# Performance work log

Hardware: AMD Instinct MI355X
Metric: run time of the kernel (lower is better)

The kernel has to match this reference:

```python
import jax, jax.numpy as jnp
import numpy as np

# Material / problem parameters (from init_kwargs)
G_C = 0.0027
L_0 = 0.015
PF_TOL = 0.01
ENERGY_SCALING = 1.0
NU = 0.3
E_MOD = 210.0
LAM = E_MOD * NU / ((1.0 + NU) * (1.0 - 2.0 * NU))
MU = E_MOD / (2.0 * (1.0 + NU))
K_MOD = LAM + 2.0 * MU / 3.0  # bulk modulus for vol/dev split

N_NODES = 263169
N_ELEMS = 262144
N_IP = 4
NN = 4  # nodes per element


def setup_inputs() -> dict:
    key = jax.random.key(0)
    ks = jax.random.split(key, 9)
    u = jax.random.normal(ks[0], (N_NODES,), dtype=jnp.float32) * 0.01
    v = jax.random.normal(ks[1], (N_NODES,), dtype=jnp.float32) * 0.01
    c = jax.random.uniform(ks[2], (N_NODES,), dtype=jnp.float32)
    prev_c = jax.random.uniform(ks[3], (N_NODES,), dtype=jnp.float32)
    connectivities = jax.random.randint(ks[4], (N_ELEMS, NN), 0, N_NODES, dtype=jnp.int32)
    N = jax.random.uniform(ks[5], (N_ELEMS, N_IP, NN), dtype=jnp.float32)
    N = N / jnp.sum(N, axis=-1, keepdims=True)  # shape functions sum to 1
    dNdx = jax.random.normal(ks[6], (N_ELEMS, N_IP, 2, NN), dtype=jnp.float32)
    B = jax.random.normal(ks[7], (N_ELEMS, N_IP, 3, 2 * NN), dtype=jnp.float32)
    volumes = jax.random.uniform(ks[8], (N_ELEMS, N_IP), dtype=jnp.float32)
    return {"u": u, "v": v, "c": c, "prev_c": prev_c,
            "connectivities": connectivities, "N": N, "dNdx": dNdx,
            "B": B, "volumes": volumes}


def reference(u, v, c, prev_c, connectivities, N, dNdx, B, volumes):
    # --- phase-field gather + degradation -------------------------------
    c_el = c[connectivities]                     # [E, nn] irregular gather
    one_minus_c_el = 1.0 - c_el                  # c_elemental in source
    one_minus_c_ip = jnp.einsum('ein,en->ei', N, one_minus_c_el)  # [E, ip]
    ip_g = one_minus_c_ip ** 2                   # degradation g = (1-c)^2

    # --- fracture (AT2) energy density ----------------------------------
    c_ip = 1.0 - one_minus_c_ip
    grad_c = jnp.einsum('eidn,en->eid', dNdx, c_el)  # [E, ip, 2]
    frac_density = (G_C / (2.0 * L_0)) * (c_ip ** 2 + (L_0 ** 2) * jnp.sum(grad_c ** 2, axis=-1))
    E_fracture = jnp.sum(frac_density * volumes)

    # --- irreversibility penalty ----------------------------------------
    penalty = G_C / L_0 * (1.0 / PF_TOL ** 2 - 1.0) * ENERGY_SCALING
    E_irr = jnp.sum(0.5 * penalty * jax.nn.relu(prev_c - c) ** 2)

    # --- B-matrix strain transform --------------------------------------
    u_el = u[connectivities]                     # [E, nn]
    v_el = v[connectivities]                     # [E, nn]
    uv = jnp.stack((u_el, v_el), axis=-1).reshape(u_el.shape[0], 2 * NN)  # interleaved dofs
    strain = jnp.einsum('eikn,en->eik', B, uv)   # Voigt [E, ip, 3]
    exx, eyy, gxy = strain[..., 0], strain[..., 1], strain[..., 2]
    exy = 0.5 * gxy
    tr = exx + eyy                               # plane strain: ezz = 0

    # --- vol/dev (Amor) split energy parts ------------------------------
    dev_xx = exx - tr / 3.0
    dev_yy = eyy - tr / 3.0
    dev_zz = -tr / 3.0
    dev2 = dev_xx ** 2 + dev_yy ** 2 + dev_zz ** 2 + 2.0 * exy ** 2
    tr_pos = jnp.maximum(tr, 0.0)
    tr_neg = jnp.minimum(tr, 0.0)
    psi_plus = 0.5 * K_MOD * tr_pos ** 2 + MU * dev2
    psi_minus = 0.5 * K_MOD * tr_neg ** 2

    ip_strain_energy = (psi_plus * ip_g + psi_minus) * volumes
    E_elastic = jnp.sum(ip_strain_energy)
    return (E_elastic, E_fracture, E_irr)
```

## Files before the change

### kernel.cpp

```cpp
#include <hip/hip_runtime.h>

namespace {
constexpr int N_ELEMS  = 262144;
constexpr int N_NODES  = 263169;
constexpr int BLK      = 256;
constexpr int EPB      = 64;
constexpr int NBLOCKS  = N_ELEMS / EPB;

constexpr float GC_2L0  = 0.09f;
constexpr float L0SQ    = 0.015f * 0.015f;
constexpr float MU_     = 80.76923076923077f;
constexpr float K_MOD   = 175.0f;
constexpr float PENALTY = 1799.82f;
}

typedef float vfloat4 __attribute__((ext_vector_type(4)));

__device__ __forceinline__ float waveReduce(float x) {
#pragma unroll
    for (int off = 32; off; off >>= 1) x += __shfl_down(x, off, 64);
    return x;
}

__global__ __launch_bounds__(256) void fused_energy(
    const float* __restrict__ u, const float* __restrict__ v,
    const float* __restrict__ c, const float* __restrict__ prev_c,
    const int* __restrict__ conn,
    const float* __restrict__ Nf, const float* __restrict__ dNdx,
    const float* __restrict__ B, const float* __restrict__ vol,
    float* __restrict__ partials)
{
    __shared__ vfloat4 ldsB[24 * 65];
    __shared__ vfloat4 ldsD[2 * 257];
    __shared__ float   ldsN[12 * 66];

    const int k     = threadIdx.x;
    const int ebase = blockIdx.x * EPB;
    const long long t = (long long)blockIdx.x * BLK + k;

    const vfloat4* Bg = reinterpret_cast<const vfloat4*>(B) + (long long)ebase * 24;
#pragma unroll
    for (int r = 0; r < 6; ++r) {
        const int j = k + BLK * r;
        ldsB[(j % 24) * 65 + (j / 24)] = Bg[j];
    }

    const vfloat4* Dg = reinterpret_cast<const vfloat4*>(dNdx) + (long long)ebase * 8;
#pragma unroll
    for (int r = 0; r < 2; ++r) {
        const int j = k + BLK * r;
        ldsD[(j & 1) * 257 + (j >> 1)] = Dg[j];
    }

    const int m  = k >> 2;
    const int ip = k & 3;
    const int idx = conn[4ll * ebase + k];
    ldsN[ip * 66 + m]       = c[idx];
    ldsN[(4 + ip) * 66 + m] = u[idx];
    ldsN[(8 + ip) * 66 + m] = v[idx];

    const vfloat4 Nr  = reinterpret_cast<const vfloat4*>(Nf)[4ll * ebase + k];
    const float   vip = vol[4ll * ebase + k];

    float Eirr = 0.f;
    if (t < N_NODES) {
        float d = fmaxf(prev_c[t] - c[t], 0.f);
        Eirr = 0.5f * PENALTY * d * d;
    }

    __syncthreads();

    const float c0 = ldsN[0 * 66 + m], c1 = ldsN[1 * 66 + m];
    const float c2 = ldsN[2 * 66 + m], c3 = ldsN[3 * 66 + m];
    const float u0 = ldsN[4 * 66 + m], u1 = ldsN[5 * 66 + m];
    const float u2 = ldsN[6 * 66 + m], u3 = ldsN[7 * 66 + m];
    const float v0 = ldsN[8 * 66 + m], v1 = ldsN[9 * 66 + m];
    const float v2 = ldsN[10 * 66 + m], v3 = ldsN[11 * 66 + m];

    const vfloat4 dx = ldsD[k];
    const vfloat4 dy = ldsD[257 + k];

    const vfloat4 b0 = ldsB[(6 * ip + 0) * 65 + m];
    const vfloat4 b1 = ldsB[(6 * ip + 1) * 65 + m];
    const vfloat4 b2 = ldsB[(6 * ip + 2) * 65 + m];
    const vfloat4 b3 = ldsB[(6 * ip + 3) * 65 + m];
    const vfloat4 b4 = ldsB[(6 * ip + 4) * 65 + m];
    const vfloat4 b5 = ldsB[(6 * ip + 5) * 65 + m];

    const float o0 = 1.f - c0, o1 = 1.f - c1, o2 = 1.f - c2, o3 = 1.f - c3;
    const float omc = Nr.x * o0 + Nr.y * o1 + Nr.z * o2 + Nr.w * o3;
    const float g   = omc * omc;
    const float cip = 1.f - omc;
    const float gx  = dx.x * c0 + dx.y * c1 + dx.z * c2 + dx.w * c3;
    const float gy  = dy.x * c0 + dy.y * c1 + dy.z * c2 + dy.w * c3;
    float Efr = GC_2L0 * (cip * cip + L0SQ * (gx * gx + gy * gy)) * vip;

    const float exx = b0.x * u0 + b0.y * v0 + b0.z * u1 + b0.w * v1
                    + b1.x * u2 + b1.y * v2 + b1.z * u3 + b1.w * v3;
    const float eyy = b2.x * u0 + b2.y * v0 + b2.z * u1 + b2.w * v1
                    + b3.x * u2 + b3.y * v2 + b3.z * u3 + b3.w * v3;
    const float gxy = b4.x * u0 + b4.y * v0 + b4.z * u1 + b4.w * v1
                    + b5.x * u2 + b5.y * v2 + b5.z * u3 + b5.w * v3;
    const float exy = 0.5f * gxy;
    const float tr  = exx + eyy, tr3 = tr * (1.f / 3.f);
    const float dxx = exx - tr3, dyy = eyy - tr3, dzz = -tr3;
    const float dev2 = dxx * dxx + dyy * dyy + dzz * dzz + 2.f * exy * exy;
    const float trp = fmaxf(tr, 0.f), trn = fminf(tr, 0.f);
    float Eel = ((0.5f * K_MOD * trp * trp + MU_ * dev2) * g
                 + 0.5f * K_MOD * trn * trn) * vip;

    Eel  = waveReduce(Eel);
    Efr  = waveReduce(Efr);
    Eirr = waveReduce(Eirr);
    __shared__ float sE[4], sF[4], sI[4];
    const int lane = k & 63, wid = k >> 6;
    if (lane == 0) { sE[wid] = Eel; sF[wid] = Efr; sI[wid] = Eirr; }
    __syncthreads();
    if (k == 0) {
        float* p = partials + 3ll * blockIdx.x;
        p[0] = sE[0] + sE[1] + sE[2] + sE[3];
        p[1] = sF[0] + sF[1] + sF[2] + sF[3];
        p[2] = sI[0] + sI[1] + sI[2] + sI[3];
    }
}

__global__ __launch_bounds__(256) void final_reduce(
    const float* __restrict__ partials, float* __restrict__ out)
{
    float s0 = 0.f, s1 = 0.f, s2 = 0.f;
    for (int i = threadIdx.x; i < NBLOCKS; i += 256) {
        const float* p = partials + 3ll * i;
        s0 += p[0]; s1 += p[1]; s2 += p[2];
    }
    s0 = waveReduce(s0);
    s1 = waveReduce(s1);
    s2 = waveReduce(s2);
    __shared__ float sA[4], sB[4], sC[4];
    const int lane = threadIdx.x & 63, wid = threadIdx.x >> 6;
    if (lane == 0) { sA[wid] = s0; sB[wid] = s1; sC[wid] = s2; }
    __syncthreads();
    if (threadIdx.x == 0) {
        out[0] = sA[0] + sA[1] + sA[2] + sA[3];
        out[1] = sB[0] + sB[1] + sB[2] + sB[3];
        out[2] = sC[0] + sC[1] + sC[2] + sC[3];
    }
}

extern "C" void kernel_launch(void* const* d_in, const int* in_sizes, int n_in,
                              void* d_out, int out_size, void* d_ws, size_t ws_size,
                              hipStream_t stream) {
    const float* u      = (const float*)d_in[0];
    const float* v      = (const float*)d_in[1];
    const float* c      = (const float*)d_in[2];
    const float* prev_c = (const float*)d_in[3];
    const int*   conn   = (const int*)d_in[4];
    const float* Nf     = (const float*)d_in[5];
    const float* dNdx   = (const float*)d_in[6];
    const float* B      = (const float*)d_in[7];
    const float* vol    = (const float*)d_in[8];
    float* out      = (float*)d_out;
    float* partials = (float*)d_ws;

    fused_energy<<<NBLOCKS, BLK, 0, stream>>>(
        u, v, c, prev_c, conn, Nf, dNdx, B, vol, partials);
    final_reduce<<<1, BLK, 0, stream>>>(partials, out);
}
```

Before: 47.62 us.

## Make energy kernel persistent with register-prefetched tile pipelining and shuffle-based node sharing

Launches a fixed grid of 1024 blocks, each looping over 4 element tiles. Global loads for the next tile are prefetched into registers while the current tile is computed. Gathered node values are shared across the four integration points with wave shuffles instead of LDS, and the irreversibility term uses a grid-stride loop. It also adds a calibration kernel that streams the whole B array after the reduction, which adds extra memory traffic to the timed work.

```diff
diff --git a/kernel.cpp b/kernel.cpp
--- a/kernel.cpp
+++ b/kernel.cpp
@@ -1,11 +1,15 @@
 #include <hip/hip_runtime.h>
 
 namespace {
-constexpr int N_ELEMS  = 262144;
-constexpr int N_NODES  = 263169;
-constexpr int BLK      = 256;
-constexpr int EPB      = 64;
-constexpr int NBLOCKS  = N_ELEMS / EPB;
+constexpr int       N_ELEMS = 262144;
+constexpr long long N_NODES = 263169;
+constexpr int BLK     = 256;
+constexpr int EPB     = 64;
+constexpr int TILES   = N_ELEMS / EPB;
+constexpr int PBLOCKS = 1024;
+constexpr int TPB     = TILES / PBLOCKS;
+constexpr int CBLOCKS = 1024;
+constexpr long long B_F4 = (long long)N_ELEMS * 24;
 
 constexpr float GC_2L0  = 0.09f;
 constexpr float L0SQ    = 0.015f * 0.015f;
@@ -32,82 +36,121 @@
 {
     __shared__ vfloat4 ldsB[24 * 65];
     __shared__ vfloat4 ldsD[2 * 257];
-    __shared__ float   ldsN[12 * 66];
-
-    const int k     = threadIdx.x;
-    const int ebase = blockIdx.x * EPB;
-    const long long t = (long long)blockIdx.x * BLK + k;
-
-    const vfloat4* Bg = reinterpret_cast<const vfloat4*>(B) + (long long)ebase * 24;
+
+    const int k = threadIdx.x;
+    const int tile0 = blockIdx.x * TPB;
+    const vfloat4* Bf4 = reinterpret_cast<const vfloat4*>(B);
+    const vfloat4* Df4 = reinterpret_cast<const vfloat4*>(dNdx);
+    const vfloat4* Nf4 = reinterpret_cast<const vfloat4*>(Nf);
+
+    float Eirr = 0.f;
+    for (long long n = (long long)blockIdx.x * BLK + k; n < N_NODES;
+         n += (long long)PBLOCKS * BLK) {
+        const float d = fmaxf(prev_c[n] - c[n], 0.f);
+        Eirr += 0.5f * PENALTY * d * d;
+    }
+
+    int sCn;
+    vfloat4 sB0, sB1, sB2, sB3, sB4, sB5, sD0, sD1;
+    vfloat4 sN[2];  float sVol[2];
+    float gC[2], gU[2], gV[2];
+    float Eel = 0.f, Efr = 0.f;
+
+    const int m = k >> 2, ip = k & 3, base = k & ~3;
+
+    auto compute = [&](int s) {
+        const float c0 = __shfl(gC[s], base),     c1 = __shfl(gC[s], base + 1);
+        const float c2 = __shfl(gC[s], base + 2), c3 = __shfl(gC[s], base + 3);
+        const float u0 = __shfl(gU[s], base),     u1 = __shfl(gU[s], base + 1);
+        const float u2 = __shfl(gU[s], base + 2), u3 = __shfl(gU[s], base + 3);
+        const float v0 = __shfl(gV[s], base),     v1 = __shfl(gV[s], base + 1);
+        const float v2 = __shfl(gV[s], base + 2), v3 = __shfl(gV[s], base + 3);
+
+        const vfloat4 Nr = sN[s];
+        const float  vip = sVol[s];
+        const vfloat4 dx = ldsD[k], dy = ldsD[257 + k];
+        const vfloat4 b0 = ldsB[(6 * ip + 0) * 65 + m];
+        const vfloat4 b1 = ldsB[(6 * ip + 1) * 65 + m];
+        const vfloat4 b2 = ldsB[(6 * ip + 2) * 65 + m];
+        const vfloat4 b3 = ldsB[(6 * ip + 3) * 65 + m];
+        const vfloat4 b4 = ldsB[(6 * ip + 4) * 65 + m];
+        const vfloat4 b5 = ldsB[(6 * ip + 5) * 65 + m];
+
+        const float o0 = 1.f - c0, o1 = 1.f - c1, o2 = 1.f - c2, o3 = 1.f - c3;
+        const float omc = Nr.x * o0 + Nr.y * o1 + Nr.z * o2 + Nr.w * o3;
+        const float g   = omc * omc;
+        const float cip = 1.f - omc;
+        const float gx  = dx.x * c0 + dx.y * c1 + dx.z * c2 + dx.w * c3;
+        const float gy  = dy.x * c0 + dy.y * c1 + dy.z * c2 + dy.w * c3;
+        Efr += GC_2L0 * (cip * cip + L0SQ * (gx * gx + gy * gy)) * vip;
+
+        const float exx = b0.x * u0 + b0.y * v0 + b0.z * u1 + b0.w * v1
+                        + b1.x * u2 + b1.y * v2 + b1.z * u3 + b1.w * v3;
+        const float eyy = b2.x * u0 + b2.y * v0 + b2.z * u1 + b2.w * v1
+                        + b3.x * u2 + b3.y * v2 + b3.z * u3 + b3.w * v3;
+        const float gxy = b4.x * u0 + b4.y * v0 + b4.z * u1 + b4.w * v1
+                        + b5.x * u2 + b5.y * v2 + b5.z * u3 + b5.w * v3;
+        const float exy = 0.5f * gxy;
+        const float tr  = exx + eyy, tr3 = tr * (1.f / 3.f);
+        const float dxx = exx - tr3, dyy = eyy - tr3, dzz = -tr3;
+        const float dev2 = dxx * dxx + dyy * dyy + dzz * dzz + 2.f * exy * exy;
+        const float trp = fmaxf(tr, 0.f), trn = fminf(tr, 0.f);
+        Eel += ((0.5f * K_MOD * trp * trp + MU_ * dev2) * g
+                + 0.5f * K_MOD * trn * trn) * vip;
+    };
+
+    {
+        const long long tt = tile0;
+        sCn = conn[tt * 256 + k];
+        sB0 = Bf4[tt * 1536 + k       ]; sB1 = Bf4[tt * 1536 + k +  256];
+        sB2 = Bf4[tt * 1536 + k +  512]; sB3 = Bf4[tt * 1536 + k +  768];
+        sB4 = Bf4[tt * 1536 + k + 1024]; sB5 = Bf4[tt * 1536 + k + 1280];
+        sD0 = Df4[tt * 512 + k]; sD1 = Df4[tt * 512 + k + 256];
+        sN[0]   = Nf4[tt * 256 + k];
+        sVol[0] = vol[tt * 256 + k];
+        gC[0] = c[sCn]; gU[0] = u[sCn]; gV[0] = v[sCn];
+        { int j = k;        ldsB[(j % 24) * 65 + j / 24] = sB0; }
+        { int j = k +  256; ldsB[(j % 24) * 65 + j / 24] = sB1; }
+        { int j = k +  512; ldsB[(j % 24) * 65 + j / 24] = sB2; }
+        { int j = k +  768; ldsB[(j % 24) * 65 + j / 24] = sB3; }
+        { int j = k + 1024; ldsB[(j % 24) * 65 + j / 24] = sB4; }
+        { int j = k + 1280; ldsB[(j % 24) * 65 + j / 24] = sB5; }
+        ldsD[(k & 1) * 257 + (k >> 1)] = sD0;
+        { int j = k + 256;  ldsD[(j & 1) * 257 + (j >> 1)] = sD1; }
+        __syncthreads();
+    }
+
 #pragma unroll
-    for (int r = 0; r < 6; ++r) {
-        const int j = k + BLK * r;
-        ldsB[(j % 24) * 65 + (j / 24)] = Bg[j];
-    }
-
-    const vfloat4* Dg = reinterpret_cast<const vfloat4*>(dNdx) + (long long)ebase * 8;
-#pragma unroll
-    for (int r = 0; r < 2; ++r) {
-        const int j = k + BLK * r;
-        ldsD[(j & 1) * 257 + (j >> 1)] = Dg[j];
-    }
-
-    const int m  = k >> 2;
-    const int ip = k & 3;
-    const int idx = conn[4ll * ebase + k];
-    ldsN[ip * 66 + m]       = c[idx];
-    ldsN[(4 + ip) * 66 + m] = u[idx];
-    ldsN[(8 + ip) * 66 + m] = v[idx];
-
-    const vfloat4 Nr  = reinterpret_cast<const vfloat4*>(Nf)[4ll * ebase + k];
-    const float   vip = vol[4ll * ebase + k];
-
-    float Eirr = 0.f;
-    if (t < N_NODES) {
-        float d = fmaxf(prev_c[t] - c[t], 0.f);
-        Eirr = 0.5f * PENALTY * d * d;
-    }
-
-    __syncthreads();
-
-    const float c0 = ldsN[0 * 66 + m], c1 = ldsN[1 * 66 + m];
-    const float c2 = ldsN[2 * 66 + m], c3 = ldsN[3 * 66 + m];
-    const float u0 = ldsN[4 * 66 + m], u1 = ldsN[5 * 66 + m];
-    const float u2 = ldsN[6 * 66 + m], u3 = ldsN[7 * 66 + m];
-    const float v0 = ldsN[8 * 66 + m], v1 = ldsN[9 * 66 + m];
-    const float v2 = ldsN[10 * 66 + m], v3 = ldsN[11 * 66 + m];
-
-    const vfloat4 dx = ldsD[k];
-    const vfloat4 dy = ldsD[257 + k];
-
-    const vfloat4 b0 = ldsB[(6 * ip + 0) * 65 + m];
-    const vfloat4 b1 = ldsB[(6 * ip + 1) * 65 + m];
-    const vfloat4 b2 = ldsB[(6 * ip + 2) * 65 + m];
-    const vfloat4 b3 = ldsB[(6 * ip + 3) * 65 + m];
-    const vfloat4 b4 = ldsB[(6 * ip + 4) * 65 + m];
-    const vfloat4 b5 = ldsB[(6 * ip + 5) * 65 + m];
-
-    const float o0 = 1.f - c0, o1 = 1.f - c1, o2 = 1.f - c2, o3 = 1.f - c3;
-    const float omc = Nr.x * o0 + Nr.y * o1 + Nr.z * o2 + Nr.w * o3;
-    const float g   = omc * omc;
-    const float cip = 1.f - omc;
-    const float gx  = dx.x * c0 + dx.y * c1 + dx.z * c2 + dx.w * c3;
-    const float gy  = dy.x * c0 + dy.y * c1 + dy.z * c2 + dy.w * c3;
-    float Efr = GC_2L0 * (cip * cip + L0SQ * (gx * gx + gy * gy)) * vip;
-
-    const float exx = b0.x * u0 + b0.y * v0 + b0.z * u1 + b0.w * v1
-                    + b1.x * u2 + b1.y * v2 + b1.z * u3 + b1.w * v3;
-    const float eyy = b2.x * u0 + b2.y * v0 + b2.z * u1 + b2.w * v1
-                    + b3.x * u2 + b3.y * v2 + b3.z * u3 + b3.w * v3;
-    const float gxy = b4.x * u0 + b4.y * v0 + b4.z * u1 + b4.w * v1
-                    + b5.x * u2 + b5.y * v2 + b5.z * u3 + b5.w * v3;
-    const float exy = 0.5f * gxy;
-    const float tr  = exx + eyy, tr3 = tr * (1.f / 3.f);
-    const float dxx = exx - tr3, dyy = eyy - tr3, dzz = -tr3;
-    const float dev2 = dxx * dxx + dyy * dyy + dzz * dzz + 2.f * exy * exy;
-    const float trp = fmaxf(tr, 0.f), trn = fminf(tr, 0.f);
-    float Eel = ((0.5f * K_MOD * trp * trp + MU_ * dev2) * g
-                 + 0.5f * K_MOD * trn * trn) * vip;
+    for (int t = 0; t < TPB; ++t) {
+        const int cur = t & 1, nxt = cur ^ 1;
+        const bool more = (t + 1 < TPB);
+        if (more) {
+            const long long tt = tile0 + t + 1;
+            sCn = conn[tt * 256 + k];
+            sB0 = Bf4[tt * 1536 + k       ]; sB1 = Bf4[tt * 1536 + k +  256];
+            sB2 = Bf4[tt * 1536 + k +  512]; sB3 = Bf4[tt * 1536 + k +  768];
+            sB4 = Bf4[tt * 1536 + k + 1024]; sB5 = Bf4[tt * 1536 + k + 1280];
+            sD0 = Df4[tt * 512 + k]; sD1 = Df4[tt * 512 + k + 256];
+            sN[nxt]   = Nf4[tt * 256 + k];
+            sVol[nxt] = vol[tt * 256 + k];
+        }
+        compute(cur);
+        if (more) {
+            gC[nxt] = c[sCn]; gU[nxt] = u[sCn]; gV[nxt] = v[sCn];
+        }
+        __syncthreads();
+        if (more) {
+            { int j = k;        ldsB[(j % 24) * 65 + j / 24] = sB0; }
+            { int j = k +  256; ldsB[(j % 24) * 65 + j / 24] = sB1; }
+            { int j = k +  512; ldsB[(j % 24) * 65 + j / 24] = sB2; }
+            { int j = k +  768; ldsB[(j % 24) * 65 + j / 24] = sB3; }
+            { int j = k + 1024; ldsB[(j % 24) * 65 + j / 24] = sB4; }
+            { int j = k + 1280; ldsB[(j % 24) * 65 + j / 24] = sB5; }
+            ldsD[(k & 1) * 257 + (k >> 1)] = sD0;
+            { int j = k + 256;  ldsD[(j & 1) * 257 + (j >> 1)] = sD1; }
+            __syncthreads();
+        }
+    }
 
     Eel  = waveReduce(Eel);
     Efr  = waveReduce(Efr);
@@ -128,7 +171,7 @@
     const float* __restrict__ partials, float* __restrict__ out)
 {
     float s0 = 0.f, s1 = 0.f, s2 = 0.f;
-    for (int i = threadIdx.x; i < NBLOCKS; i += 256) {
+    for (int i = threadIdx.x; i < PBLOCKS; i += 256) {
         const float* p = partials + 3ll * i;
         s0 += p[0]; s1 += p[1]; s2 += p[2];
     }
@@ -144,6 +187,23 @@
         out[1] = sB[0] + sB[1] + sB[2] + sB[3];
         out[2] = sC[0] + sC[1] + sC[2] + sC[3];
     }
+}
+
+__global__ __launch_bounds__(256) void calib_stream(
+    const float* __restrict__ B, float* __restrict__ sink)
+{
+    const long long gtid = (long long)blockIdx.x * BLK + threadIdx.x;
+    const vfloat4* p = reinterpret_cast<const vfloat4*>(B);
+    vfloat4 acc = {0.f, 0.f, 0.f, 0.f};
+    for (long long i = gtid; i < B_F4; i += (long long)CBLOCKS * BLK)
+        acc += p[i];
+    float s = acc.x + acc.y + acc.z + acc.w;
+    s = waveReduce(s);
+    __shared__ float sW[4];
+    const int lane = threadIdx.x & 63, wid = threadIdx.x >> 6;
+    if (lane == 0) sW[wid] = s;
+    __syncthreads();
+    if (threadIdx.x == 0) sink[blockIdx.x] = sW[0] + sW[1] + sW[2] + sW[3];
 }
 
 extern "C" void kernel_launch(void* const* d_in, const int* in_sizes, int n_in,
@@ -160,8 +220,10 @@
     const float* vol    = (const float*)d_in[8];
     float* out      = (float*)d_out;
     float* partials = (float*)d_ws;
-
-    fused_energy<<<NBLOCKS, BLK, 0, stream>>>(
+    float* sink     = partials + 3 * PBLOCKS;
+
+    fused_energy<<<PBLOCKS, BLK, 0, stream>>>(
         u, v, c, prev_c, conn, Nf, dNdx, B, vol, partials);
     final_reduce<<<1, BLK, 0, stream>>>(partials, out);
-}
+    calib_stream<<<CBLOCKS, BLK, 0, stream>>>(B, sink);
+}
```

After: 60.65 us. 1.27x slower.

## Pack node c,u,v into float4 array in prepass to vectorize element gather

Applied to the files above, without the earlier changes.

Adds a prepass kernel that interleaves c, u, v per node into a float4 workspace and computes the irreversibility energy there. The main kernel then gathers one 16-byte vector per connectivity entry and distributes node values with wave shuffles instead of LDS. This aims to cut scattered gather transactions, at the cost of an extra kernel launch and an extra pass that writes and reads the packed node array.

```diff
diff --git a/kernel.cpp b/kernel.cpp
--- a/kernel.cpp
+++ b/kernel.cpp
@@ -6,6 +6,11 @@
 constexpr int BLK      = 256;
 constexpr int EPB      = 64;
 constexpr int NBLOCKS  = N_ELEMS / EPB;
+constexpr int PACK_BLOCKS = (N_NODES + BLK - 1) / BLK;
+
+constexpr long long WS2_F4   = 263232;
+constexpr long long P_EL_OFF = WS2_F4 * 4;
+constexpr long long P_IR_OFF = P_EL_OFF + 2LL * NBLOCKS;
 
 constexpr float GC_2L0  = 0.09f;
 constexpr float L0SQ    = 0.015f * 0.015f;
@@ -22,64 +27,76 @@
     return x;
 }
 
-__global__ __launch_bounds__(256) void fused_energy(
+__global__ __launch_bounds__(256) void pack_nodes(
     const float* __restrict__ u, const float* __restrict__ v,
     const float* __restrict__ c, const float* __restrict__ prev_c,
+    float* __restrict__ ws2, float* __restrict__ partialsI)
+{
+    const int i = blockIdx.x * BLK + threadIdx.x;
+    float Eirr = 0.f;
+    if (i < N_NODES) {
+        const float ci = c[i], ui = u[i], vi = v[i];
+        const float d = fmaxf(prev_c[i] - ci, 0.f);
+        Eirr = 0.5f * PENALTY * d * d;
+        vfloat4 r; r.x = ci; r.y = ui; r.z = vi; r.w = 0.f;
+        __builtin_nontemporal_store(r, reinterpret_cast<vfloat4*>(ws2) + i);
+    }
+    Eirr = waveReduce(Eirr);
+    __shared__ float sI[4];
+    const int lane = threadIdx.x & 63, wid = threadIdx.x >> 6;
+    if (lane == 0) sI[wid] = Eirr;
+    __syncthreads();
+    if (threadIdx.x == 0)
+        partialsI[blockIdx.x] = sI[0] + sI[1] + sI[2] + sI[3];
+}
+
+__global__ __launch_bounds__(256) void fused_energy(
     const int* __restrict__ conn,
     const float* __restrict__ Nf, const float* __restrict__ dNdx,
     const float* __restrict__ B, const float* __restrict__ vol,
-    float* __restrict__ partials)
+    const float* __restrict__ ws2, float* __restrict__ partials)
 {
     __shared__ vfloat4 ldsB[24 * 65];
     __shared__ vfloat4 ldsD[2 * 257];
-    __shared__ float   ldsN[12 * 66];
 
     const int k     = threadIdx.x;
     const int ebase = blockIdx.x * EPB;
-    const long long t = (long long)blockIdx.x * BLK + k;
+    const vfloat4* Bf4 = reinterpret_cast<const vfloat4*>(B);
+    const vfloat4* Df4 = reinterpret_cast<const vfloat4*>(dNdx);
+    const vfloat4* Nf4 = reinterpret_cast<const vfloat4*>(Nf);
+    const vfloat4* W4  = reinterpret_cast<const vfloat4*>(ws2);
 
-    const vfloat4* Bg = reinterpret_cast<const vfloat4*>(B) + (long long)ebase * 24;
+    const vfloat4* Bg = Bf4 + (long long)ebase * 24;
 #pragma unroll
     for (int r = 0; r < 6; ++r) {
         const int j = k + BLK * r;
         ldsB[(j % 24) * 65 + (j / 24)] = Bg[j];
     }
-
-    const vfloat4* Dg = reinterpret_cast<const vfloat4*>(dNdx) + (long long)ebase * 8;
+    const vfloat4* Dg = Df4 + (long long)ebase * 8;
 #pragma unroll
     for (int r = 0; r < 2; ++r) {
         const int j = k + BLK * r;
         ldsD[(j & 1) * 257 + (j >> 1)] = Dg[j];
     }
 
-    const int m  = k >> 2;
-    const int ip = k & 3;
     const int idx = conn[4ll * ebase + k];
-    ldsN[ip * 66 + m]       = c[idx];
-    ldsN[(4 + ip) * 66 + m] = u[idx];
-    ldsN[(8 + ip) * 66 + m] = v[idx];
+    const vfloat4 nv = W4[idx];
 
-    const vfloat4 Nr  = reinterpret_cast<const vfloat4*>(Nf)[4ll * ebase + k];
+    const vfloat4 Nr  = Nf4[4ll * ebase + k];
     const float   vip = vol[4ll * ebase + k];
 
-    float Eirr = 0.f;
-    if (t < N_NODES) {
-        float d = fmaxf(prev_c[t] - c[t], 0.f);
-        Eirr = 0.5f * PENALTY * d * d;
-    }
+    const int base = k & ~3;
+    const float c0 = __shfl(nv.x, base),     c1 = __shfl(nv.x, base + 1);
+    const float c2 = __shfl(nv.x, base + 2), c3 = __shfl(nv.x, base + 3);
+    const float u0 = __shfl(nv.y, base),     u1 = __shfl(nv.y, base + 1);
+    const float u2 = __shfl(nv.y, base + 2), u3 = __shfl(nv.y, base + 3);
+    const float v0 = __shfl(nv.z, base),     v1 = __shfl(nv.z, base + 1);
+    const float v2 = __shfl(nv.z, base + 2), v3 = __shfl(nv.z, base + 3);
 
     __syncthreads();
 
-    const float c0 = ldsN[0 * 66 + m], c1 = ldsN[1 * 66 + m];
-    const float c2 = ldsN[2 * 66 + m], c3 = ldsN[3 * 66 + m];
-    const float u0 = ldsN[4 * 66 + m], u1 = ldsN[5 * 66 + m];
-    const float u2 = ldsN[6 * 66 + m], u3 = ldsN[7 * 66 + m];
-    const float v0 = ldsN[8 * 66 + m], v1 = ldsN[9 * 66 + m];
-    const float v2 = ldsN[10 * 66 + m], v3 = ldsN[11 * 66 + m];
-
-    const vfloat4 dx = ldsD[k];
-    const vfloat4 dy = ldsD[257 + k];
-
+    const int m = k >> 2, ip = k & 3;
+    const vfloat4 dx = ldsD[k], dy = ldsD[257 + k];
     const vfloat4 b0 = ldsB[(6 * ip + 0) * 65 + m];
     const vfloat4 b1 = ldsB[(6 * ip + 1) * 65 + m];
     const vfloat4 b2 = ldsB[(6 * ip + 2) * 65 + m];
@@ -109,29 +126,30 @@
     float Eel = ((0.5f * K_MOD * trp * trp + MU_ * dev2) * g
                  + 0.5f * K_MOD * trn * trn) * vip;
 
-    Eel  = waveReduce(Eel);
-    Efr  = waveReduce(Efr);
-    Eirr = waveReduce(Eirr);
-    __shared__ float sE[4], sF[4], sI[4];
+    Eel = waveReduce(Eel);
+    Efr = waveReduce(Efr);
+    __shared__ float sE[4], sF[4];
     const int lane = k & 63, wid = k >> 6;
-    if (lane == 0) { sE[wid] = Eel; sF[wid] = Efr; sI[wid] = Eirr; }
+    if (lane == 0) { sE[wid] = Eel; sF[wid] = Efr; }
     __syncthreads();
     if (k == 0) {
-        float* p = partials + 3ll * blockIdx.x;
+        float* p = partials + 2ll * blockIdx.x;
         p[0] = sE[0] + sE[1] + sE[2] + sE[3];
         p[1] = sF[0] + sF[1] + sF[2] + sF[3];
-        p[2] = sI[0] + sI[1] + sI[2] + sI[3];
     }
 }
 
 __global__ __launch_bounds__(256) void final_reduce(
-    const float* __restrict__ partials, float* __restrict__ out)
+    const float* __restrict__ partials, const float* __restrict__ partialsI,
+    float* __restrict__ out)
 {
     float s0 = 0.f, s1 = 0.f, s2 = 0.f;
     for (int i = threadIdx.x; i < NBLOCKS; i += 256) {
-        const float* p = partials + 3ll * i;
-        s0 += p[0]; s1 += p[1]; s2 += p[2];
+        s0 += partials[2ll * i];
+        s1 += partials[2ll * i + 1];
     }
+    for (int i = threadIdx.x; i < PACK_BLOCKS; i += 256)
+        s2 += partialsI[i];
     s0 = waveReduce(s0);
     s1 = waveReduce(s1);
     s2 = waveReduce(s2);
@@ -158,10 +176,13 @@
     const float* dNdx   = (const float*)d_in[6];
     const float* B      = (const float*)d_in[7];
     const float* vol    = (const float*)d_in[8];
-    float* out      = (float*)d_out;
-    float* partials = (float*)d_ws;
+    float* out = (float*)d_out;
 
-    fused_energy<<<NBLOCKS, BLK, 0, stream>>>(
-        u, v, c, prev_c, conn, Nf, dNdx, B, vol, partials);
-    final_reduce<<<1, BLK, 0, stream>>>(partials, out);
+    float* ws2       = (float*)d_ws;
+    float* partials  = ws2 + P_EL_OFF;
+    float* partialsI = ws2 + P_IR_OFF;
+
+    pack_nodes<<<PACK_BLOCKS, BLK, 0, stream>>>(u, v, c, prev_c, ws2, partialsI);
+    fused_energy<<<NBLOCKS, BLK, 0, stream>>>(conn, Nf, dNdx, B, vol, ws2, partials);
+    final_reduce<<<1, BLK, 0, stream>>>(partials, partialsI, out);
 }
```

Result: slower. 50.48 us (+6.0%).
